# Kernel optimization log

Hardware: AMD Instinct MI355X
Metric: run time of the kernel (lower is better)

Reference implementation:

```python
import jax, jax.numpy as jnp
import numpy as np

B, S, D, H = 4, 2048, 1024, 16
HD = D // H  # head_dim = 64


def setup_inputs() -> dict:
    key = jax.random.key(0)
    ks = jax.random.split(key, 14)
    s = 0.02
    return {
        "inputs_q": jax.random.normal(ks[0], (B, S, D), jnp.float32),
        "pos_emb_q": jax.random.normal(ks[1], (1, S, D), jnp.float32),
        "pos_emb_k": jax.random.normal(ks[2], (1, S, D), jnp.float32),
        "pos_emb_v": jax.random.normal(ks[3], (1, S, D), jnp.float32),
        "attention_bias": jax.random.normal(ks[4], (1, 1, S, S), jnp.float32),
        "attention_bias_kv": jax.random.normal(ks[5], (B, S), jnp.float32),
        "wq": jax.random.normal(ks[6], (D, H, HD), jnp.float32) * s,
        "bq": jnp.zeros((H, HD), jnp.float32),
        "wk": jax.random.normal(ks[7], (D, H, HD), jnp.float32) * s,
        "bk": jnp.zeros((H, HD), jnp.float32),
        "wv": jax.random.normal(ks[8], (D, H, HD), jnp.float32) * s,
        "bv": jnp.zeros((H, HD), jnp.float32),
        "wo": jax.random.normal(ks[9], (H, HD, D), jnp.float32) * s,
        "bo": jnp.zeros((D,), jnp.float32),
    }


def reference(inputs_q, pos_emb_q, pos_emb_k, pos_emb_v, attention_bias,
              attention_bias_kv, wq, bq, wk, bk, wv, bv, wo, bo):
    # Self-attention: inputs_kv = inputs_q. Additive pos-embs BEFORE projection.
    q_in = inputs_q + pos_emb_q
    k_in = inputs_q + pos_emb_k
    v_in = inputs_q + pos_emb_v
    # QKV DenseGeneral: [B,S,D] -> [B,S,H,HD]
    q = jnp.einsum('bsd,dhk->bshk', q_in, wq) + bq
    k = jnp.einsum('bsd,dhk->bshk', k_in, wk) + bk
    v = jnp.einsum('bsd,dhk->bshk', v_in, wv) + bv
    # Scaled dot-product attention with full bias + key-only bias.
    q = q / jnp.sqrt(jnp.asarray(HD, q.dtype))
    scores = jnp.einsum('bqhk,bshk->bhqs', q, k)  # [B,H,Sq,Sk]
    scores = scores + attention_bias + attention_bias_kv[:, None, None, :]
    attn = jax.nn.softmax(scores, axis=-1)
    x = jnp.einsum('bhqs,bshk->bqhk', attn, v)  # [B,S,H,HD]
    # Output projection contracting (H, HD) -> D.
    out = jnp.einsum('bqhk,hkd->bqd', x, wo) + bo
    return out
```

## Files before the change

### kernel.cpp

```cpp
#include <hip/hip_runtime.h>

typedef __attribute__((ext_vector_type(8))) short short8;
typedef __attribute__((ext_vector_type(4))) float f32x4;

#define MFMA16(a, b, c) __builtin_amdgcn_mfma_f32_16x16x32_bf16(a, b, c, 0, 0, 0)

#define SEQ 2048
#define DIM 1024
#define NH 16
#define HD 64
#define LOG2E 1.4426950408889634f

__device__ __forceinline__ ushort f2bf(float f) {
  union { float f; unsigned u; } v; v.f = f;
  unsigned r = (v.u + 0x7FFFu + ((v.u >> 16) & 1u)) >> 16;
  return (ushort)r;
}

__device__ __forceinline__ ushort bf1(float f) {
  unsigned r;
  asm("v_cvt_pk_bf16_f32 %0, %1, %2" : "=v"(r) : "v"(f), "v"(f));
  return (ushort)(r & 0xffffu);
}

__device__ __forceinline__ float exp2fn(float x) {
#if __has_builtin(__builtin_amdgcn_exp2f)
  return __builtin_amdgcn_exp2f(x);
#else
  return exp2f(x);
#endif
}

__global__ __launch_bounds__(256) void prep_a(
    const float* __restrict__ x, const float* __restrict__ pq,
    const float* __restrict__ pk, const float* __restrict__ pv,
    ushort* __restrict__ aq, ushort* __restrict__ ak, ushort* __restrict__ av) {
  int i = (blockIdx.x * 256 + threadIdx.x) * 4;
  int pi = i & (SEQ * DIM - 1);
  float4 xv = *(const float4*)(x + i);
  float4 q4 = *(const float4*)(pq + pi);
  float4 k4 = *(const float4*)(pk + pi);
  float4 v4 = *(const float4*)(pv + pi);
  ushort4 o;
  o.x = f2bf(xv.x + q4.x); o.y = f2bf(xv.y + q4.y);
  o.z = f2bf(xv.z + q4.z); o.w = f2bf(xv.w + q4.w);
  *(ushort4*)(aq + i) = o;
  o.x = f2bf(xv.x + k4.x); o.y = f2bf(xv.y + k4.y);
  o.z = f2bf(xv.z + k4.z); o.w = f2bf(xv.w + k4.w);
  *(ushort4*)(ak + i) = o;
  o.x = f2bf(xv.x + v4.x); o.y = f2bf(xv.y + v4.y);
  o.z = f2bf(xv.z + v4.z); o.w = f2bf(xv.w + v4.w);
  *(ushort4*)(av + i) = o;
}

__global__ __launch_bounds__(256) void transpose_all(
    const float* __restrict__ w0, const float* __restrict__ w1,
    const float* __restrict__ w2, const float* __restrict__ w3,
    ushort* __restrict__ d0, ushort* __restrict__ d1,
    ushort* __restrict__ d2, ushort* __restrict__ d3) {
  const int z = blockIdx.z;
  const float* src = z == 0 ? w0 : z == 1 ? w1 : z == 2 ? w2 : w3;
  ushort* dst = z == 0 ? d0 : z == 1 ? d1 : z == 2 ? d2 : d3;
  __shared__ float t[32][33];
  int tx = threadIdx.x & 31, ty = threadIdx.x >> 5;
  int x0 = blockIdx.x * 32, y0 = blockIdx.y * 32;
#pragma unroll
  for (int j = 0; j < 32; j += 8) t[ty + j][tx] = src[(size_t)(y0 + ty + j) * DIM + x0 + tx];
  __syncthreads();
#pragma unroll
  for (int j = 0; j < 32; j += 8)
    dst[(size_t)(x0 + ty + j) * DIM + y0 + tx] = f2bf(t[tx][ty + j]);
}

__global__ __launch_bounds__(256) void gemm_qkv(
    const ushort* __restrict__ aq, const ushort* __restrict__ ak,
    const ushort* __restrict__ av, const ushort* __restrict__ wqT,
    const ushort* __restrict__ wkT, const ushort* __restrict__ wvT,
    const float* __restrict__ bq, const float* __restrict__ bk,
    const float* __restrict__ bv, ushort* __restrict__ Qb,
    ushort* __restrict__ Kb, ushort* __restrict__ VTb) {
  constexpr int K = 1024, LDA = 40;
  __shared__ __align__(16) ushort As[128 * LDA];
  __shared__ __align__(16) ushort Bs[128 * LDA];
  const int proj = blockIdx.y >> 3, bn = blockIdx.y & 7, bm = blockIdx.x;
  const ushort* A = proj == 0 ? aq : proj == 1 ? ak : av;
  const ushort* Bt = proj == 0 ? wqT : proj == 1 ? wkT : wvT;
  const float* bias = proj == 0 ? bq : proj == 1 ? bk : bv;
  ushort* outp = proj == 0 ? Qb : proj == 1 ? Kb : VTb;
  const float scale = proj == 0 ? 0.125f * LOG2E : 1.0f;

  const int tid = threadIdx.x;
  const int wave = tid >> 6, lane = tid & 63;
  const int wr = wave >> 1, wc = wave & 1;
  const int g = lane >> 4, l15 = lane & 15;
  const int r0 = tid >> 2, c0 = (tid & 3) * 8;
  const ushort* Ap = A + (size_t)(bm * 128 + r0) * K + c0;
  const ushort* Bp = Bt + (size_t)(bn * 128 + r0) * K + c0;
  f32x4 acc[4][4] = {};

  uint4 ra0 = *(const uint4*)(Ap);
  uint4 ra1 = *(const uint4*)(Ap + (size_t)64 * K);
  uint4 rb0 = *(const uint4*)(Bp);
  uint4 rb1 = *(const uint4*)(Bp + (size_t)64 * K);

  for (int kt = 0; kt < K; kt += 32) {
    __syncthreads();
    *(uint4*)&As[r0 * LDA + c0] = ra0;
    *(uint4*)&As[(r0 + 64) * LDA + c0] = ra1;
    *(uint4*)&Bs[r0 * LDA + c0] = rb0;
    *(uint4*)&Bs[(r0 + 64) * LDA + c0] = rb1;
    __syncthreads();
    if (kt + 32 < K) {
      ra0 = *(const uint4*)(Ap + kt + 32);
      ra1 = *(const uint4*)(Ap + (size_t)64 * K + kt + 32);
      rb0 = *(const uint4*)(Bp + kt + 32);
      rb1 = *(const uint4*)(Bp + (size_t)64 * K + kt + 32);
    }
    short8 af[4], bfr[4];
#pragma unroll
    for (int m = 0; m < 4; ++m)
      af[m] = *(const short8*)&As[(wr * 64 + m * 16 + l15) * LDA + g * 8];
#pragma unroll
    for (int n = 0; n < 4; ++n)
      bfr[n] = *(const short8*)&Bs[(wc * 64 + n * 16 + l15) * LDA + g * 8];
#pragma unroll
    for (int m = 0; m < 4; ++m)
#pragma unroll
      for (int n = 0; n < 4; ++n) acc[m][n] = MFMA16(af[m], bfr[n], acc[m][n]);
  }

#pragma unroll
  for (int m = 0; m < 4; ++m) {
    int row = bm * 128 + wr * 64 + m * 16 + g * 4;
#pragma unroll
    for (int n = 0; n < 4; ++n) {
      int col = bn * 128 + wc * 64 + n * 16 + l15;
      float bv2 = bias[col];
#pragma unroll
      for (int j = 0; j < 4; ++j) {
        float v = (acc[m][n][j] + bv2) * scale;
        int r = row + j;
        int b = r >> 11, s = r & (SEQ - 1), h = col >> 6, hd = col & (HD - 1);
        if (proj < 2)
          outp[((size_t)((b * NH + h) * SEQ + s)) * HD + hd] = f2bf(v);
        else
          outp[((size_t)((b * NH + h) * HD + hd)) * SEQ + s] = f2bf(v);
      }
    }
  }
}

__global__ __launch_bounds__(256) void gemm_out(
    const ushort* __restrict__ A, const ushort* __restrict__ Bt,
    const float* __restrict__ bias, float* __restrict__ outp) {
  constexpr int K = 1024, LDA = 40;
  __shared__ __align__(16) ushort As[128 * LDA];
  __shared__ __align__(16) ushort Bs[128 * LDA];
  const int tid = threadIdx.x;
  const int wave = tid >> 6, lane = tid & 63;
  const int wr = wave >> 1, wc = wave & 1;
  const int g = lane >> 4, l15 = lane & 15;
  const int bm = blockIdx.x, bn = blockIdx.y;
  const int r0 = tid >> 2, c0 = (tid & 3) * 8;
  const ushort* Ap = A + (size_t)(bm * 128 + r0) * K + c0;
  const ushort* Bp = Bt + (size_t)(bn * 128 + r0) * K + c0;
  f32x4 acc[4][4] = {};

  uint4 ra0 = *(const uint4*)(Ap);
  uint4 ra1 = *(const uint4*)(Ap + (size_t)64 * K);
  uint4 rb0 = *(const uint4*)(Bp);
  uint4 rb1 = *(const uint4*)(Bp + (size_t)64 * K);

  for (int kt = 0; kt < K; kt += 32) {
    __syncthreads();
    *(uint4*)&As[r0 * LDA + c0] = ra0;
    *(uint4*)&As[(r0 + 64) * LDA + c0] = ra1;
    *(uint4*)&Bs[r0 * LDA + c0] = rb0;
    *(uint4*)&Bs[(r0 + 64) * LDA + c0] = rb1;
    __syncthreads();
    if (kt + 32 < K) {
      ra0 = *(const uint4*)(Ap + kt + 32);
      ra1 = *(const uint4*)(Ap + (size_t)64 * K + kt + 32);
      rb0 = *(const uint4*)(Bp + kt + 32);
      rb1 = *(const uint4*)(Bp + (size_t)64 * K + kt + 32);
    }
    short8 af[4], bfr[4];
#pragma unroll
    for (int m = 0; m < 4; ++m)
      af[m] = *(const short8*)&As[(wr * 64 + m * 16 + l15) * LDA + g * 8];
#pragma unroll
    for (int n = 0; n < 4; ++n)
      bfr[n] = *(const short8*)&Bs[(wc * 64 + n * 16 + l15) * LDA + g * 8];
#pragma unroll
    for (int m = 0; m < 4; ++m)
#pragma unroll
      for (int n = 0; n < 4; ++n) acc[m][n] = MFMA16(af[m], bfr[n], acc[m][n]);
  }

#pragma unroll
  for (int m = 0; m < 4; ++m) {
    int row = bm * 128 + wr * 64 + m * 16 + g * 4;
#pragma unroll
    for (int n = 0; n < 4; ++n) {
      int col = bn * 128 + wc * 64 + n * 16 + l15;
      float bv = bias[col];
#pragma unroll
      for (int j = 0; j < 4; ++j)
        outp[(size_t)(row + j) * DIM + col] = acc[m][n][j] + bv;
    }
  }
}

__global__ __launch_bounds__(256) void attn10(
    const ushort* __restrict__ Q, const ushort* __restrict__ K,
    const ushort* __restrict__ VT, const float* __restrict__ abias,
    const float* __restrict__ kvbias, ushort* __restrict__ X) {
  constexpr int LDK = 72, LDV = 72, LDP = 72;
  __shared__ __align__(16) ushort Ks[64 * LDK];
  __shared__ __align__(16) ushort Vs[64 * LDV];
  __shared__ __align__(16) ushort Ps[4][16 * LDP];
  const int tid = threadIdx.x;
  const int w = tid >> 6, lane = tid & 63, g = lane >> 4, l15 = lane & 15;
  const int px = blockIdx.x;
  const int bh = px & 63;
  const int qt = px >> 6;
  const int b = bh >> 4, h = bh & (NH - 1);
  const int q0 = qt * 64;

  short8 qf[2];
  {
    const ushort* qp = Q + ((size_t)bh * SEQ + q0 + w * 16 + l15) * HD;
#pragma unroll
    for (int c = 0; c < 2; ++c) qf[c] = *(const short8*)(qp + c * 32 + g * 8);
  }

  f32x4 o[4] = {};
  float l_lane[4] = {};

  const int sr = tid >> 2, scc = (tid & 3) * 16;
  const ushort* Kp = K + (size_t)bh * SEQ * HD;
  const ushort* Vp = VT + (size_t)bh * HD * SEQ;
  const float* abp = abias + (size_t)q0 * SEQ;
  const float* kvp = kvbias + b * SEQ;

  uint4 ka = *(const uint4*)(Kp + (size_t)sr * HD + scc);
  uint4 kb = *(const uint4*)(Kp + (size_t)sr * HD + scc + 8);
  uint4 va = *(const uint4*)(Vp + (size_t)sr * SEQ + scc);
  uint4 vb = *(const uint4*)(Vp + (size_t)sr * SEQ + scc + 8);

  for (int kt = 0; kt < SEQ / 64; ++kt) {
    const int k0 = kt * 64;
    __syncthreads();
    *(uint4*)&Ks[sr * LDK + scc] = ka;
    *(uint4*)&Ks[sr * LDK + scc + 8] = kb;
    *(uint4*)&Vs[sr * LDV + scc] = va;
    *(uint4*)&Vs[sr * LDV + scc + 8] = vb;
    __syncthreads();

    float bkv[4];
#pragma unroll
    for (int ct = 0; ct < 4; ++ct) bkv[ct] = kvp[k0 + ct * 16 + l15];
    float abf[4][4];
#pragma unroll
    for (int j = 0; j < 4; ++j) {
      const float* abr = abp + (size_t)(w * 16 + 4 * g + j) * SEQ + k0 + l15;
#pragma unroll
      for (int ct = 0; ct < 4; ++ct) abf[ct][j] = abr[ct * 16];
    }

    if (kt + 1 < SEQ / 64) {
      ka = *(const uint4*)(Kp + (size_t)(k0 + 64 + sr) * HD + scc);
      kb = *(const uint4*)(Kp + (size_t)(k0 + 64 + sr) * HD + scc + 8);
      va = *(const uint4*)(Vp + (size_t)sr * SEQ + k0 + 64 + scc);
      vb = *(const uint4*)(Vp + (size_t)sr * SEQ + k0 + 64 + scc + 8);
    }

    f32x4 s4[4];
#pragma unroll
    for (int ct = 0; ct < 4; ++ct) {
      short8 kf0 = *(const short8*)&Ks[(ct * 16 + l15) * LDK + g * 8];
      short8 kf1 = *(const short8*)&Ks[(ct * 16 + l15) * LDK + 32 + g * 8];
      f32x4 z = {0.f, 0.f, 0.f, 0.f};
      f32x4 t = MFMA16(qf[0], kf0, z);
      s4[ct] = MFMA16(qf[1], kf1, t);
    }

    {
      float p[4][4];
#pragma unroll
      for (int ct = 0; ct < 4; ++ct)
#pragma unroll
        for (int j = 0; j < 4; ++j)
          p[ct][j] = exp2fn(fmaf(abf[ct][j] + bkv[ct], LOG2E, s4[ct][j]));
#pragma unroll
      for (int j = 0; j < 4; ++j)
        l_lane[j] += (p[0][j] + p[1][j]) + (p[2][j] + p[3][j]);
#pragma unroll
      for (int ct = 0; ct < 4; ++ct)
#pragma unroll
        for (int j = 0; j < 4; ++j)
          Ps[w][(4 * g + j) * LDP + ct * 16 + l15] = bf1(p[ct][j]);
    }

    asm volatile("s_waitcnt lgkmcnt(0)" ::: "memory");
    __builtin_amdgcn_sched_barrier(0);

    short8 pa[2];
#pragma unroll
    for (int ks = 0; ks < 2; ++ks)
      pa[ks] = *(const short8*)&Ps[w][l15 * LDP + ks * 32 + g * 8];
#pragma unroll
    for (int ctd = 0; ctd < 4; ++ctd) {
      short8 vf0 = *(const short8*)&Vs[(ctd * 16 + l15) * LDV + g * 8];
      short8 vf1 = *(const short8*)&Vs[(ctd * 16 + l15) * LDV + 32 + g * 8];
      o[ctd] = MFMA16(pa[0], vf0, o[ctd]);
      o[ctd] = MFMA16(pa[1], vf1, o[ctd]);
    }
  }

  float inv[4];
#pragma unroll
  for (int j = 0; j < 4; ++j) {
    float l = l_lane[j];
    l += __shfl_xor(l, 1);
    l += __shfl_xor(l, 2);
    l += __shfl_xor(l, 4);
    l += __shfl_xor(l, 8);
    inv[j] = 1.0f / l;
  }
#pragma unroll
  for (int ctd = 0; ctd < 4; ++ctd)
#pragma unroll
    for (int j = 0; j < 4; ++j) {
      size_t row = (size_t)b * SEQ + q0 + w * 16 + 4 * g + j;
      X[row * DIM + h * HD + ctd * 16 + l15] = bf1(o[ctd][j] * inv[j]);
    }
}

extern "C" void kernel_launch(void* const* d_in, const int* in_sizes, int n_in,
                              void* d_out, int out_size, void* d_ws, size_t ws_size,
                              hipStream_t stream) {
  const float* inputs_q = (const float*)d_in[0];
  const float* pos_q = (const float*)d_in[1];
  const float* pos_k = (const float*)d_in[2];
  const float* pos_v = (const float*)d_in[3];
  const float* abias = (const float*)d_in[4];
  const float* kvbias = (const float*)d_in[5];
  const float* wq = (const float*)d_in[6];
  const float* bq = (const float*)d_in[7];
  const float* wk = (const float*)d_in[8];
  const float* bk = (const float*)d_in[9];
  const float* wv = (const float*)d_in[10];
  const float* bv = (const float*)d_in[11];
  const float* wo = (const float*)d_in[12];
  const float* bo = (const float*)d_in[13];

  char* ws = (char*)d_ws;
  const size_t MB = 1ull << 20;
  ushort* wqT = (ushort*)(ws + 0 * MB);
  ushort* wkT = (ushort*)(ws + 2 * MB);
  ushort* wvT = (ushort*)(ws + 4 * MB);
  ushort* woT = (ushort*)(ws + 6 * MB);
  ushort* aq = (ushort*)(ws + 8 * MB);
  ushort* ak = (ushort*)(ws + 24 * MB);
  ushort* av = (ushort*)(ws + 40 * MB);
  ushort* Qb = (ushort*)(ws + 56 * MB);
  ushort* Kb = (ushort*)(ws + 72 * MB);
  ushort* VTb = (ushort*)(ws + 88 * MB);
  ushort* Xb = (ushort*)(ws + 8 * MB);

  prep_a<<<8192, 256, 0, stream>>>(inputs_q, pos_q, pos_k, pos_v, aq, ak, av);
  transpose_all<<<dim3(32, 32, 4), 256, 0, stream>>>(wq, wk, wv, wo, wqT, wkT, wvT, woT);
  gemm_qkv<<<dim3(64, 24), 256, 0, stream>>>(aq, ak, av, wqT, wkT, wvT,
                                             bq, bk, bv, Qb, Kb, VTb);
  attn10<<<2048, 256, 0, stream>>>(Qb, Kb, VTb, abias, kvbias, Xb);
  gemm_out<<<dim3(64, 8), 256, 0, stream>>>(Xb, woT, bo, (float*)d_out);
}
```

Measured before the change: 290.0 us.

## Load K and V MFMA fragments directly from global memory, dropping LDS staging

Result: slower. 630.7 us (+117.5%).

```diff
diff --git a/kernel.cpp b/kernel.cpp
--- a/kernel.cpp
+++ b/kernel.cpp
@@ -211,13 +211,11 @@
   }
 }
 
-__global__ __launch_bounds__(256) void attn10(
+__global__ __launch_bounds__(256) void attn11(
     const ushort* __restrict__ Q, const ushort* __restrict__ K,
     const ushort* __restrict__ VT, const float* __restrict__ abias,
     const float* __restrict__ kvbias, ushort* __restrict__ X) {
-  constexpr int LDK = 72, LDV = 72, LDP = 72;
-  __shared__ __align__(16) ushort Ks[64 * LDK];
-  __shared__ __align__(16) ushort Vs[64 * LDV];
+  constexpr int LDP = 72;
   __shared__ __align__(16) ushort Ps[4][16 * LDP];
   const int tid = threadIdx.x;
   const int w = tid >> 6, lane = tid & 63, g = lane >> 4, l15 = lane & 15;
@@ -237,26 +235,24 @@
   f32x4 o[4] = {};
   float l_lane[4] = {};
 
-  const int sr = tid >> 2, scc = (tid & 3) * 16;
   const ushort* Kp = K + (size_t)bh * SEQ * HD;
   const ushort* Vp = VT + (size_t)bh * HD * SEQ;
   const float* abp = abias + (size_t)q0 * SEQ;
   const float* kvp = kvbias + b * SEQ;
 
-  uint4 ka = *(const uint4*)(Kp + (size_t)sr * HD + scc);
-  uint4 kb = *(const uint4*)(Kp + (size_t)sr * HD + scc + 8);
-  uint4 va = *(const uint4*)(Vp + (size_t)sr * SEQ + scc);
-  uint4 vb = *(const uint4*)(Vp + (size_t)sr * SEQ + scc + 8);
+  const ushort* Kl = Kp + (size_t)l15 * HD + g * 8;
+  const ushort* Vl = Vp + (size_t)l15 * SEQ + g * 8;
 
   for (int kt = 0; kt < SEQ / 64; ++kt) {
     const int k0 = kt * 64;
-    __syncthreads();
-    *(uint4*)&Ks[sr * LDK + scc] = ka;
-    *(uint4*)&Ks[sr * LDK + scc + 8] = kb;
-    *(uint4*)&Vs[sr * LDV + scc] = va;
-    *(uint4*)&Vs[sr * LDV + scc + 8] = vb;
-    __syncthreads();
-
+
+    short8 kf[4][2];
+#pragma unroll
+    for (int ct = 0; ct < 4; ++ct) {
+      const ushort* kr = Kl + (size_t)(k0 + ct * 16) * HD;
+      kf[ct][0] = *(const short8*)(kr);
+      kf[ct][1] = *(const short8*)(kr + 32);
+    }
     float bkv[4];
 #pragma unroll
     for (int ct = 0; ct < 4; ++ct) bkv[ct] = kvp[k0 + ct * 16 + l15];
@@ -268,21 +264,20 @@
       for (int ct = 0; ct < 4; ++ct) abf[ct][j] = abr[ct * 16];
     }
 
-    if (kt + 1 < SEQ / 64) {
-      ka = *(const uint4*)(Kp + (size_t)(k0 + 64 + sr) * HD + scc);
-      kb = *(const uint4*)(Kp + (size_t)(k0 + 64 + sr) * HD + scc + 8);
-      va = *(const uint4*)(Vp + (size_t)sr * SEQ + k0 + 64 + scc);
-      vb = *(const uint4*)(Vp + (size_t)sr * SEQ + k0 + 64 + scc + 8);
-    }
-
     f32x4 s4[4];
 #pragma unroll
     for (int ct = 0; ct < 4; ++ct) {
-      short8 kf0 = *(const short8*)&Ks[(ct * 16 + l15) * LDK + g * 8];
-      short8 kf1 = *(const short8*)&Ks[(ct * 16 + l15) * LDK + 32 + g * 8];
       f32x4 z = {0.f, 0.f, 0.f, 0.f};
-      f32x4 t = MFMA16(qf[0], kf0, z);
-      s4[ct] = MFMA16(qf[1], kf1, t);
+      f32x4 t = MFMA16(qf[0], kf[ct][0], z);
+      s4[ct] = MFMA16(qf[1], kf[ct][1], t);
+    }
+
+    short8 vf[4][2];
+#pragma unroll
+    for (int ctd = 0; ctd < 4; ++ctd) {
+      const ushort* vr = Vl + (size_t)(ctd * 16) * SEQ + k0;
+      vf[ctd][0] = *(const short8*)(vr);
+      vf[ctd][1] = *(const short8*)(vr + 32);
     }
 
     {
@@ -311,10 +306,8 @@
       pa[ks] = *(const short8*)&Ps[w][l15 * LDP + ks * 32 + g * 8];
 #pragma unroll
     for (int ctd = 0; ctd < 4; ++ctd) {
-      short8 vf0 = *(const short8*)&Vs[(ctd * 16 + l15) * LDV + g * 8];
-      short8 vf1 = *(const short8*)&Vs[(ctd * 16 + l15) * LDV + 32 + g * 8];
-      o[ctd] = MFMA16(pa[0], vf0, o[ctd]);
-      o[ctd] = MFMA16(pa[1], vf1, o[ctd]);
+      o[ctd] = MFMA16(pa[0], vf[ctd][0], o[ctd]);
+      o[ctd] = MFMA16(pa[1], vf[ctd][1], o[ctd]);
     }
   }
 
@@ -373,6 +366,6 @@
   transpose_all<<<dim3(32, 32, 4), 256, 0, stream>>>(wq, wk, wv, wo, wqT, wkT, wvT, woT);
   gemm_qkv<<<dim3(64, 24), 256, 0, stream>>>(aq, ak, av, wqT, wkT, wvT,
                                              bq, bk, bv, Qb, Kb, VTb);
-  attn10<<<2048, 256, 0, stream>>>(Qb, Kb, VTb, abias, kvbias, Xb);
+  attn11<<<2048, 256, 0, stream>>>(Qb, Kb, VTb, abias, kvbias, Xb);
   gemm_out<<<dim3(64, 8), 256, 0, stream>>>(Xb, woT, bo, (float*)d_out);
 }
```
